# Kernel optimization log

Measured on AMD Instinct MI355X. Metric: run time of the kernel, lower is better.

The kernel has to match this reference:

```python
import jax, jax.numpy as jnp
import numpy as np

B, CIN, COUT, H, W = 64, 2048, 32, 14, 14
REP = 1024


def setup_inputs() -> dict:
    key = jax.random.key(0)
    ks = jax.random.split(key, 7)
    x = jax.random.normal(ks[0], (B, CIN, H, W), dtype=jnp.float32)
    conv_w = jax.random.normal(ks[1], (COUT, CIN, 3, 3), dtype=jnp.float32) * (1.0 / np.sqrt(CIN * 9))
    conv_b = jax.random.normal(ks[2], (COUT,), dtype=jnp.float32) * 0.01
    w6 = jax.random.normal(ks[3], (REP, CIN * COUT), dtype=jnp.float32) * (1.0 / np.sqrt(CIN * COUT))
    b6 = jax.random.normal(ks[4], (REP,), dtype=jnp.float32) * 0.01
    w7 = jax.random.normal(ks[5], (REP, REP), dtype=jnp.float32) * (1.0 / np.sqrt(REP))
    b7 = jax.random.normal(ks[6], (REP,), dtype=jnp.float32) * 0.01
    return {"x": x, "conv_w": conv_w, "conv_b": conv_b,
            "w6": w6, "b6": b6, "w7": w7, "b7": b7}


def reference(x, conv_w, conv_b, w6, b6, w7, b7):
    # attention_map = Conv2d(in->out, k=3, s=1, p=1)(x)  -> [B, COUT, H, W]
    am = jax.lax.conv_general_dilated(
        x, conv_w, window_strides=(1, 1), padding=((1, 1), (1, 1)),
        dimension_numbers=("NCHW", "OIHW", "NCHW"))
    am = am + conv_b[None, :, None, None]
    # outer product am[:,None]*x[:,:,None] followed by AdaptiveAvgPool2d(1)
    # == mean over HW of the product: [B, CIN, COUT]
    hw = x.shape[2] * x.shape[3]
    pooled = jnp.einsum("bihw,bohw->bio", x, am) / hw
    feat = pooled.reshape(pooled.shape[0], -1)          # [B, CIN*COUT]
    h6 = jax.nn.relu(feat @ w6.T + b6)                  # [B, REP]
    out = jax.nn.relu(h6 @ w7.T + b7)                   # [B, REP]
    return out
```

## Files before the change

kernel.cpp:

```cpp
#include <hip/hip_runtime.h>
#include <hip/hip_bf16.h>

#define B_   64
#define CIN  2048
#define COUT 32
#define P    196
#define PPAD 224
#define REP  1024
#define K1   (CIN*COUT)
#define NSL  16

typedef float  f32x4  __attribute__((ext_vector_type(4)));
typedef __bf16 bf16x8 __attribute__((ext_vector_type(8)));
typedef __bf16 bf16x4 __attribute__((ext_vector_type(4)));

#define OFF_W2     0
#define OFF_AMP    1179648
#define OFF_AMBF   30539776
#define OFF_POOLED 31457280
#define OFF_S1     39845888
#define OFF_H6B    48234496
#define OFF_S2     48365568

static __device__ __forceinline__ f32x4 mfma16(bf16x8 a, bf16x8 b, f32x4 c) {
  return __builtin_amdgcn_mfma_f32_16x16x32_bf16(a, b, c, 0, 0, 0);
}

__global__ __launch_bounds__(256)
void prep_w2(const float* __restrict__ cw, __bf16* __restrict__ W2) {
  const int blk = blockIdx.x;
  const int o = blk >> 3, cc = blk & 7;
  const int cin = cc * 256 + threadIdx.x;
  const float* src = cw + ((size_t)o * CIN + cin) * 9;
  #pragma unroll
  for (int d = 0; d < 9; d++)
    W2[((size_t)d * COUT + o) * CIN + cin] = (__bf16)src[d];
}

#define ICW 72
__global__ __launch_bounds__(448)
void conv_kernel(const float* __restrict__ x, const __bf16* __restrict__ W2,
                 float* __restrict__ amp) {
  __shared__ __bf16 XT[256 * ICW];

  const int ksl = blockIdx.x;
  const int bb  = blockIdx.y;
  const int t   = threadIdx.x;
  const int wv  = t >> 6;
  const int lane = t & 63;
  const int q = lane >> 4, ln = lane & 15;
  const float* xb = x + (size_t)bb * CIN * P;
  const int kbase = ksl * 128;

  int rb[2]; bool valid[2]; int pix[2];
  #pragma unroll
  for (int nt = 0; nt < 2; nt++) {
    const int pt = wv * 32 + nt * 16 + ln;
    pix[nt] = pt; valid[nt] = (pt < P);
    const int pr = valid[nt] ? pt : 0;
    const int h = pr / 14, w = pr - (pr / 14) * 14;
    rb[nt] = (h + 1) * 16 + (w + 1);
  }
  f32x4 acc[2][2];
  #pragma unroll
  for (int m = 0; m < 2; m++)
    #pragma unroll
    for (int n = 0; n < 2; n++) { f32x4 z = {0.f,0.f,0.f,0.f}; acc[m][n] = z; }

  const int nIter = (t < 224) ? 4 : 3;
  int obase[4], dst[4];
  #pragma unroll
  for (int it = 0; it < 4; it++) {
    const int u = t + 448 * it;
    if (u < 1568) {
      const int g = u / 196, p = u - g * 196;
      const int h = p / 14, w = p - (p / 14) * 14;
      obase[it] = (g * 8) * P + p;
      dst[it]   = ((h + 1) * 16 + (w + 1)) * ICW + g * 8;
    } else { obase[it] = 0; dst[it] = 0; }
  }

  bf16x8 pre[4];
  #pragma unroll
  for (int it = 0; it < 4; it++)
    if (it < nIter) {
      bf16x8 v;
      #pragma unroll
      for (int j = 0; j < 8; j++)
        v[j] = (__bf16)xb[(size_t)kbase * P + obase[it] + j * P];
      pre[it] = v;
    }

  if (t < 256) {
    const int hh = t >> 4, ww = t & 15;
    if (hh == 0 || hh == 15 || ww == 0 || ww == 15) {
      #pragma unroll
      for (int g = 0; g < 8; g++) { bf16x8 z = {}; *(bf16x8*)&XT[t * ICW + g * 8] = z; }
    }
  }

  #pragma unroll
  for (int it = 0; it < 4; it++)
    if (it < nIter) *(bf16x8*)&XT[dst[it]] = pre[it];

  #pragma unroll
  for (int it = 0; it < 4; it++)
    if (it < nIter) {
      bf16x8 v;
      #pragma unroll
      for (int j = 0; j < 8; j++)
        v[j] = (__bf16)xb[(size_t)(kbase + 64) * P + obase[it] + j * P];
      pre[it] = v;
    }

  __syncthreads();

  #pragma unroll
  for (int sub = 0; sub < 2; sub++) {
    const int i0 = kbase + sub * 64;
    #pragma unroll
    for (int ks2 = 0; ks2 < 2; ks2++) {
      const int kg  = i0 + ks2 * 32 + q * 8;
      const int off = (ks2 * 4 + q) * 8;
      #pragma unroll
      for (int d = 0; d < 9; d++) {
        const int dy = d / 3, dx = d - (d / 3) * 3;
        const int delta = (dy - 1) * 16 + (dx - 1);
        bf16x8 a0 = *(const bf16x8*)&W2[(size_t)(d * COUT + ln) * CIN + kg];
        bf16x8 a1 = *(const bf16x8*)&W2[(size_t)(d * COUT + 16 + ln) * CIN + kg];
        #pragma unroll
        for (int nt = 0; nt < 2; nt++) {
          bf16x8 bf = *(const bf16x8*)&XT[(rb[nt] + delta) * ICW + off];
          acc[0][nt] = mfma16(a0, bf, acc[0][nt]);
          acc[1][nt] = mfma16(a1, bf, acc[1][nt]);
        }
      }
    }
    if (sub == 0) {
      __syncthreads();
      #pragma unroll
      for (int it = 0; it < 4; it++)
        if (it < nIter) *(bf16x8*)&XT[dst[it]] = pre[it];
      __syncthreads();
    }
  }

  float* dstp = amp + (((size_t)ksl * B_ + bb) * COUT) * PPAD;
  #pragma unroll
  for (int mt = 0; mt < 2; mt++)
    #pragma unroll
    for (int nt = 0; nt < 2; nt++)
      if (valid[nt]) {
        #pragma unroll
        for (int r = 0; r < 4; r++) {
          const int o = mt * 16 + q * 4 + r;
          dstp[(size_t)o * PPAD + pix[nt]] = acc[mt][nt][r];
        }
      }
}

__global__ __launch_bounds__(256)
void am_final_kernel(const float* __restrict__ amp, const float* __restrict__ cb,
                     __bf16* __restrict__ am_bf) {
  const int NE = B_ * COUT * PPAD;
  for (int e = blockIdx.x * 256 + threadIdx.x; e < NE; e += 448 * 256) {
    const int row = e / PPAD;
    const int pe  = e - row * PPAD;
    float v = 0.f;
    if (pe < P) {
      float s = 0.f;
      #pragma unroll
      for (int sl = 0; sl < NSL; sl++) s += amp[(size_t)sl * NE + e];
      v = s + cb[row & (COUT - 1)];
    }
    am_bf[e] = (__bf16)v;
  }
}

__global__ __launch_bounds__(256)
void pooled_kernel(const float* __restrict__ x, const __bf16* __restrict__ amb_,
                   __bf16* __restrict__ pooled) {
  const int b  = blockIdx.y;
  const int ig = blockIdx.x;
  const int t  = threadIdx.x;
  const int wv = t >> 6;
  const int lane = t & 63;
  const int q = lane >> 4, ln = lane & 15;
  const int ibase = ig * 128 + wv * 32;

  f32x4 acc[2][2];
  #pragma unroll
  for (int a = 0; a < 2; a++)
    #pragma unroll
    for (int c = 0; c < 2; c++) { f32x4 z = {0.f,0.f,0.f,0.f}; acc[a][c] = z; }

  const __bf16* amb = amb_ + (size_t)b * COUT * PPAD;
  const float*  xb  = x + (size_t)b * CIN * P;

  #pragma unroll
  for (int kc = 0; kc < 7; kc++) {
    const int k0 = kc * 32 + q * 8;
    bf16x8 af[2];
    #pragma unroll
    for (int o2 = 0; o2 < 2; o2++)
      af[o2] = *(const bf16x8*)&amb[(size_t)(o2 * 16 + ln) * PPAD + k0];
    #pragma unroll
    for (int it = 0; it < 2; it++) {
      const int i = ibase + it * 16 + ln;
      bf16x8 bfr;
      if (kc < 6) {
        const float* src = &xb[(size_t)i * P + k0];
        f32x4 v0 = *(const f32x4*)src;
        f32x4 v1 = *(const f32x4*)(src + 4);
        #pragma unroll
        for (int j = 0; j < 4; j++) { bfr[j] = (__bf16)v0[j]; bfr[4 + j] = (__bf16)v1[j]; }
      } else {
        #pragma unroll
        for (int j = 0; j < 8; j++) {
          const int p = k0 + j;
          bfr[j] = (p < P) ? (__bf16)xb[(size_t)i * P + p] : (__bf16)0.f;
        }
      }
      acc[0][it] = mfma16(af[0], bfr, acc[0][it]);
      acc[1][it] = mfma16(af[1], bfr, acc[1][it]);
    }
  }

  const float sc = 1.0f / 196.0f;
  #pragma unroll
  for (int o2 = 0; o2 < 2; o2++)
    #pragma unroll
    for (int it = 0; it < 2; it++) {
      const int i = ibase + it * 16 + ln;
      bf16x4 vv;
      #pragma unroll
      for (int r = 0; r < 4; r++) vv[r] = (__bf16)(acc[o2][it][r] * sc);
      *(bf16x4*)&pooled[(size_t)b * K1 + (size_t)i * COUT + o2 * 16 + q * 4] = vv;
    }
}

__global__ __launch_bounds__(256)
void gemm1_kernel(const __bf16* __restrict__ pooled, const float* __restrict__ w6,
                  float* __restrict__ S1) {
  const int nb = blockIdx.x, ks = blockIdx.y;
  const int t = threadIdx.x;
  const int wv = t >> 6;
  const int lane = t & 63;
  const int q = lane >> 4, ln = lane & 15;
  const int n0 = nb * 64 + wv * 16;
  const int kbase = ks * 2048;

  f32x4 acc[4];
  #pragma unroll
  for (int a = 0; a < 4; a++) { f32x4 z = {0.f,0.f,0.f,0.f}; acc[a] = z; }

  #pragma unroll 4
  for (int kc = 0; kc < 64; kc++) {
    const int k0 = kbase + kc * 32 + q * 8;
    const float* src = &w6[(size_t)(n0 + ln) * K1 + k0];
    f32x4 v0 = *(const f32x4*)src;
    f32x4 v1 = *(const f32x4*)(src + 4);
    bf16x8 bfr;
    #pragma unroll
    for (int j = 0; j < 4; j++) { bfr[j] = (__bf16)v0[j]; bfr[4 + j] = (__bf16)v1[j]; }
    #pragma unroll
    for (int mi = 0; mi < 4; mi++) {
      bf16x8 af = *(const bf16x8*)&pooled[(size_t)(mi * 16 + ln) * K1 + k0];
      acc[mi] = mfma16(af, bfr, acc[mi]);
    }
  }
  #pragma unroll
  for (int mi = 0; mi < 4; mi++)
    #pragma unroll
    for (int r = 0; r < 4; r++)
      S1[(size_t)ks * (B_ * REP) + (size_t)(mi * 16 + q * 4 + r) * REP + n0 + ln] = acc[mi][r];
}

__global__ __launch_bounds__(256)
void reduce1_kernel(const float* __restrict__ S1, const float* __restrict__ b6,
                    __bf16* __restrict__ h6b) {
  const int idx = blockIdx.x * 256 + threadIdx.x;
  float s = 0.f;
  #pragma unroll 8
  for (int ks = 0; ks < 32; ks++) s += S1[(size_t)ks * (B_ * REP) + idx];
  h6b[idx] = (__bf16)fmaxf(s + b6[idx & (REP - 1)], 0.f);
}

__global__ __launch_bounds__(256)
void gemm2_kernel(const __bf16* __restrict__ h6b, const float* __restrict__ w7,
                  float* __restrict__ S2) {
  const int nb = blockIdx.x, ks = blockIdx.y;
  const int t = threadIdx.x;
  const int wv = t >> 6;
  const int lane = t & 63;
  const int q = lane >> 4, ln = lane & 15;
  const int n0 = nb * 64 + wv * 16;

  f32x4 acc[4];
  #pragma unroll
  for (int a = 0; a < 4; a++) { f32x4 z = {0.f,0.f,0.f,0.f}; acc[a] = z; }

  #pragma unroll
  for (int kc = 0; kc < 4; kc++) {
    const int k0 = ks * 128 + kc * 32 + q * 8;
    const float* src = &w7[(size_t)(n0 + ln) * REP + k0];
    f32x4 v0 = *(const f32x4*)src;
    f32x4 v1 = *(const f32x4*)(src + 4);
    bf16x8 bfr;
    #pragma unroll
    for (int j = 0; j < 4; j++) { bfr[j] = (__bf16)v0[j]; bfr[4 + j] = (__bf16)v1[j]; }
    #pragma unroll
    for (int mi = 0; mi < 4; mi++) {
      bf16x8 af = *(const bf16x8*)&h6b[(size_t)(mi * 16 + ln) * REP + k0];
      acc[mi] = mfma16(af, bfr, acc[mi]);
    }
  }
  #pragma unroll
  for (int mi = 0; mi < 4; mi++)
    #pragma unroll
    for (int r = 0; r < 4; r++)
      S2[(size_t)ks * (B_ * REP) + (size_t)(mi * 16 + q * 4 + r) * REP + n0 + ln] = acc[mi][r];
}

__global__ __launch_bounds__(256)
void reduce2_kernel(const float* __restrict__ S2, const float* __restrict__ b7,
                    float* __restrict__ out) {
  const int idx = blockIdx.x * 256 + threadIdx.x;
  float s = 0.f;
  #pragma unroll
  for (int ks = 0; ks < 8; ks++) s += S2[(size_t)ks * (B_ * REP) + idx];
  out[idx] = fmaxf(s + b7[idx & (REP - 1)], 0.f);
}

extern "C" void kernel_launch(void* const* d_in, const int* in_sizes, int n_in,
                              void* d_out, int out_size, void* d_ws, size_t ws_size,
                              hipStream_t stream) {
  const float* x   = (const float*)d_in[0];
  const float* cw  = (const float*)d_in[1];
  const float* cb  = (const float*)d_in[2];
  const float* w6  = (const float*)d_in[3];
  const float* b6  = (const float*)d_in[4];
  const float* w7  = (const float*)d_in[5];
  const float* b7  = (const float*)d_in[6];
  float* out = (float*)d_out;

  char* ws = (char*)d_ws;
  __bf16* W2     = (__bf16*)(ws + OFF_W2);
  float*  amp    = (float*)(ws + OFF_AMP);
  __bf16* am_bf  = (__bf16*)(ws + OFF_AMBF);
  __bf16* pooled = (__bf16*)(ws + OFF_POOLED);
  float*  S1     = (float*)(ws + OFF_S1);
  __bf16* h6b    = (__bf16*)(ws + OFF_H6B);
  float*  S2     = (float*)(ws + OFF_S2);

  prep_w2        <<<256,          256, 0, stream>>>(cw, W2);
  conv_kernel    <<<dim3(16, 64), 448, 0, stream>>>(x, W2, amp);
  am_final_kernel<<<448,          256, 0, stream>>>(amp, cb, am_bf);
  pooled_kernel  <<<dim3(16, 64), 256, 0, stream>>>(x, am_bf, pooled);
  gemm1_kernel   <<<dim3(16, 32), 256, 0, stream>>>(pooled, w6, S1);
  reduce1_kernel <<<256,          256, 0, stream>>>(S1, b6, h6b);
  gemm2_kernel   <<<dim3(16, 8),  256, 0, stream>>>(h6b, w7, S2);
  reduce2_kernel <<<256,          256, 0, stream>>>(S2, b7, out);
}
```

Measured before the change: 572.7 us.

## Load full conv K-slice at once, double gemm1 split-K, fuse gemm2 reduction

The conv kernel now stages all 128 input channels of its slice into a wider LDS tile in one pass, dropping the two-phase double-buffer and its extra barriers. gemm1 uses 64 K-splits instead of 32 for more parallelism, and reduce1 reads the larger partial buffer. gemm2 drops split-K, does the full K loop per block, and applies bias and ReLU directly, which removes reduce2 and the S2 buffer. The trade-offs are more LDS per conv block, lower occupancy, and only 16 blocks for gemm2.

```diff
diff --git a/kernel.cpp b/kernel.cpp
--- a/kernel.cpp
+++ b/kernel.cpp
@@ -19,8 +19,7 @@
 #define OFF_AMBF   30539776
 #define OFF_POOLED 31457280
 #define OFF_S1     39845888
-#define OFF_H6B    48234496
-#define OFF_S2     48365568
+#define OFF_H6B    56623104
 
 static __device__ __forceinline__ f32x4 mfma16(bf16x8 a, bf16x8 b, f32x4 c) {
   return __builtin_amdgcn_mfma_f32_16x16x32_bf16(a, b, c, 0, 0, 0);
@@ -37,11 +36,11 @@
     W2[((size_t)d * COUT + o) * CIN + cin] = (__bf16)src[d];
 }
 
-#define ICW 72
+#define ICW2 136
 __global__ __launch_bounds__(448)
 void conv_kernel(const float* __restrict__ x, const __bf16* __restrict__ W2,
                  float* __restrict__ amp) {
-  __shared__ __bf16 XT[256 * ICW];
+  __shared__ __bf16 XT[256 * ICW2];
 
   const int ksl = blockIdx.x;
   const int bb  = blockIdx.y;
@@ -67,81 +66,63 @@
     #pragma unroll
     for (int n = 0; n < 2; n++) { f32x4 z = {0.f,0.f,0.f,0.f}; acc[m][n] = z; }
 
-  const int nIter = (t < 224) ? 4 : 3;
-  int obase[4], dst[4];
+  int obase[7], dst[7];
+  #pragma unroll
+  for (int it = 0; it < 7; it++) {
+    const int u = t + 448 * it;
+    const int g = u / 196, p = u - g * 196;
+    const int h = p / 14, w = p - (p / 14) * 14;
+    obase[it] = (kbase + g * 8) * P + p;
+    dst[it]   = ((h + 1) * 16 + (w + 1)) * ICW2 + g * 8;
+  }
+
+  bf16x8 pre[4];
   #pragma unroll
   for (int it = 0; it < 4; it++) {
-    const int u = t + 448 * it;
-    if (u < 1568) {
-      const int g = u / 196, p = u - g * 196;
-      const int h = p / 14, w = p - (p / 14) * 14;
-      obase[it] = (g * 8) * P + p;
-      dst[it]   = ((h + 1) * 16 + (w + 1)) * ICW + g * 8;
-    } else { obase[it] = 0; dst[it] = 0; }
-  }
-
-  bf16x8 pre[4];
-  #pragma unroll
-  for (int it = 0; it < 4; it++)
-    if (it < nIter) {
-      bf16x8 v;
-      #pragma unroll
-      for (int j = 0; j < 8; j++)
-        v[j] = (__bf16)xb[(size_t)kbase * P + obase[it] + j * P];
-      pre[it] = v;
-    }
-
+    bf16x8 v;
+    #pragma unroll
+    for (int j = 0; j < 8; j++) v[j] = (__bf16)xb[obase[it] + j * P];
+    pre[it] = v;
+  }
   if (t < 256) {
     const int hh = t >> 4, ww = t & 15;
     if (hh == 0 || hh == 15 || ww == 0 || ww == 15) {
       #pragma unroll
-      for (int g = 0; g < 8; g++) { bf16x8 z = {}; *(bf16x8*)&XT[t * ICW + g * 8] = z; }
-    }
-  }
-
-  #pragma unroll
-  for (int it = 0; it < 4; it++)
-    if (it < nIter) *(bf16x8*)&XT[dst[it]] = pre[it];
-
-  #pragma unroll
-  for (int it = 0; it < 4; it++)
-    if (it < nIter) {
-      bf16x8 v;
+      for (int g = 0; g < 16; g++) { bf16x8 z = {}; *(bf16x8*)&XT[t * ICW2 + g * 8] = z; }
+    }
+  }
+  #pragma unroll
+  for (int it = 0; it < 4; it++) *(bf16x8*)&XT[dst[it]] = pre[it];
+
+  bf16x8 pre2[3];
+  #pragma unroll
+  for (int it = 0; it < 3; it++) {
+    bf16x8 v;
+    #pragma unroll
+    for (int j = 0; j < 8; j++) v[j] = (__bf16)xb[obase[4 + it] + j * P];
+    pre2[it] = v;
+  }
+  #pragma unroll
+  for (int it = 0; it < 3; it++) *(bf16x8*)&XT[dst[4 + it]] = pre2[it];
+
+  __syncthreads();
+
+  #pragma unroll
+  for (int ks2 = 0; ks2 < 4; ks2++) {
+    const int kg  = kbase + ks2 * 32 + q * 8;
+    const int off = (ks2 * 4 + q) * 8;
+    #pragma unroll
+    for (int d = 0; d < 9; d++) {
+      const int dy = d / 3, dx = d - (d / 3) * 3;
+      const int delta = (dy - 1) * 16 + (dx - 1);
+      bf16x8 a0 = *(const bf16x8*)&W2[(size_t)(d * COUT + ln) * CIN + kg];
+      bf16x8 a1 = *(const bf16x8*)&W2[(size_t)(d * COUT + 16 + ln) * CIN + kg];
       #pragma unroll
-      for (int j = 0; j < 8; j++)
-        v[j] = (__bf16)xb[(size_t)(kbase + 64) * P + obase[it] + j * P];
-      pre[it] = v;
-    }
-
-  __syncthreads();
-
-  #pragma unroll
-  for (int sub = 0; sub < 2; sub++) {
-    const int i0 = kbase + sub * 64;
-    #pragma unroll
-    for (int ks2 = 0; ks2 < 2; ks2++) {
-      const int kg  = i0 + ks2 * 32 + q * 8;
-      const int off = (ks2 * 4 + q) * 8;
-      #pragma unroll
-      for (int d = 0; d < 9; d++) {
-        const int dy = d / 3, dx = d - (d / 3) * 3;
-        const int delta = (dy - 1) * 16 + (dx - 1);
-        bf16x8 a0 = *(const bf16x8*)&W2[(size_t)(d * COUT + ln) * CIN + kg];
-        bf16x8 a1 = *(const bf16x8*)&W2[(size_t)(d * COUT + 16 + ln) * CIN + kg];
-        #pragma unroll
-        for (int nt = 0; nt < 2; nt++) {
-          bf16x8 bf = *(const bf16x8*)&XT[(rb[nt] + delta) * ICW + off];
-          acc[0][nt] = mfma16(a0, bf, acc[0][nt]);
-          acc[1][nt] = mfma16(a1, bf, acc[1][nt]);
-        }
+      for (int nt = 0; nt < 2; nt++) {
+        bf16x8 bf = *(const bf16x8*)&XT[(rb[nt] + delta) * ICW2 + off];
+        acc[0][nt] = mfma16(a0, bf, acc[0][nt]);
+        acc[1][nt] = mfma16(a1, bf, acc[1][nt]);
       }
-    }
-    if (sub == 0) {
-      __syncthreads();
-      #pragma unroll
-      for (int it = 0; it < 4; it++)
-        if (it < nIter) *(bf16x8*)&XT[dst[it]] = pre[it];
-      __syncthreads();
     }
   }
 
@@ -248,14 +229,14 @@
   const int lane = t & 63;
   const int q = lane >> 4, ln = lane & 15;
   const int n0 = nb * 64 + wv * 16;
-  const int kbase = ks * 2048;
+  const int kbase = ks * 1024;
 
   f32x4 acc[4];
   #pragma unroll
   for (int a = 0; a < 4; a++) { f32x4 z = {0.f,0.f,0.f,0.f}; acc[a] = z; }
 
   #pragma unroll 4
-  for (int kc = 0; kc < 64; kc++) {
+  for (int kc = 0; kc < 32; kc++) {
     const int k0 = kbase + kc * 32 + q * 8;
     const float* src = &w6[(size_t)(n0 + ln) * K1 + k0];
     f32x4 v0 = *(const f32x4*)src;
@@ -282,14 +263,14 @@
   const int idx = blockIdx.x * 256 + threadIdx.x;
   float s = 0.f;
   #pragma unroll 8
-  for (int ks = 0; ks < 32; ks++) s += S1[(size_t)ks * (B_ * REP) + idx];
+  for (int ks = 0; ks < 64; ks++) s += S1[(size_t)ks * (B_ * REP) + idx];
   h6b[idx] = (__bf16)fmaxf(s + b6[idx & (REP - 1)], 0.f);
 }
 
 __global__ __launch_bounds__(256)
 void gemm2_kernel(const __bf16* __restrict__ h6b, const float* __restrict__ w7,
-                  float* __restrict__ S2) {
-  const int nb = blockIdx.x, ks = blockIdx.y;
+                  const float* __restrict__ b7, float* __restrict__ out) {
+  const int nb = blockIdx.x;
   const int t = threadIdx.x;
   const int wv = t >> 6;
   const int lane = t & 63;
@@ -300,9 +281,9 @@
   #pragma unroll
   for (int a = 0; a < 4; a++) { f32x4 z = {0.f,0.f,0.f,0.f}; acc[a] = z; }
 
-  #pragma unroll
-  for (int kc = 0; kc < 4; kc++) {
-    const int k0 = ks * 128 + kc * 32 + q * 8;
+  #pragma unroll 4
+  for (int kc = 0; kc < 32; kc++) {
+    const int k0 = kc * 32 + q * 8;
     const float* src = &w7[(size_t)(n0 + ln) * REP + k0];
     f32x4 v0 = *(const f32x4*)src;
     f32x4 v1 = *(const f32x4*)(src + 4);
@@ -315,21 +296,13 @@
       acc[mi] = mfma16(af, bfr, acc[mi]);
     }
   }
+
+  const float bias = b7[n0 + ln];
   #pragma unroll
   for (int mi = 0; mi < 4; mi++)
     #pragma unroll
     for (int r = 0; r < 4; r++)
-      S2[(size_t)ks * (B_ * REP) + (size_t)(mi * 16 + q * 4 + r) * REP + n0 + ln] = acc[mi][r];
-}
-
-__global__ __launch_bounds__(256)
-void reduce2_kernel(const float* __restrict__ S2, const float* __restrict__ b7,
-                    float* __restrict__ out) {
-  const int idx = blockIdx.x * 256 + threadIdx.x;
-  float s = 0.f;
-  #pragma unroll
-  for (int ks = 0; ks < 8; ks++) s += S2[(size_t)ks * (B_ * REP) + idx];
-  out[idx] = fmaxf(s + b7[idx & (REP - 1)], 0.f);
+      out[(size_t)(mi * 16 + q * 4 + r) * REP + n0 + ln] = fmaxf(acc[mi][r] + bias, 0.f);
 }
 
 extern "C" void kernel_launch(void* const* d_in, const int* in_sizes, int n_in,
@@ -351,14 +324,12 @@
   __bf16* pooled = (__bf16*)(ws + OFF_POOLED);
   float*  S1     = (float*)(ws + OFF_S1);
   __bf16* h6b    = (__bf16*)(ws + OFF_H6B);
-  float*  S2     = (float*)(ws + OFF_S2);
 
   prep_w2        <<<256,          256, 0, stream>>>(cw, W2);
   conv_kernel    <<<dim3(16, 64), 448, 0, stream>>>(x, W2, amp);
   am_final_kernel<<<448,          256, 0, stream>>>(amp, cb, am_bf);
   pooled_kernel  <<<dim3(16, 64), 256, 0, stream>>>(x, am_bf, pooled);
-  gemm1_kernel   <<<dim3(16, 32), 256, 0, stream>>>(pooled, w6, S1);
+  gemm1_kernel   <<<dim3(16, 64), 256, 0, stream>>>(pooled, w6, S1);
   reduce1_kernel <<<256,          256, 0, stream>>>(S1, b6, h6b);
-  gemm2_kernel   <<<dim3(16, 8),  256, 0, stream>>>(h6b, w7, S2);
-  reduce2_kernel <<<256,          256, 0, stream>>>(S2, b7, out);
-}
+  gemm2_kernel   <<<16,           256, 0, stream>>>(h6b, w7, b7, out);
+}
```

After: 600.9 us. +4.9%, slower.

## Replace conv split-K partial buffer with atomics and fuse reductions into consumers

Applied to the files above, without the earlier changes.

Conv slices now atomically accumulate into a single zeroed activation map instead of writing 16 partial copies, so the separate reduction kernel is removed and the bias is added inside the pooling kernel. The second GEMM drops its K split and applies bias and ReLU directly, eliminating the final reduction kernel. This cuts large intermediate memory traffic and two launches, at the cost of atomic contention and a much smaller grid for the second GEMM.

```diff
diff --git a/kernel.cpp b/kernel.cpp
--- a/kernel.cpp
+++ b/kernel.cpp
@@ -15,12 +15,10 @@
 typedef __bf16 bf16x4 __attribute__((ext_vector_type(4)));
 
 #define OFF_W2     0
-#define OFF_AMP    1179648
-#define OFF_AMBF   30539776
-#define OFF_POOLED 31457280
-#define OFF_S1     39845888
-#define OFF_H6B    48234496
-#define OFF_S2     48365568
+#define OFF_AM     1310720
+#define OFF_POOLED 3145728
+#define OFF_S1     11534336
+#define OFF_H6B    19922944
 
 static __device__ __forceinline__ f32x4 mfma16(bf16x8 a, bf16x8 b, f32x4 c) {
   return __builtin_amdgcn_mfma_f32_16x16x32_bf16(a, b, c, 0, 0, 0);
@@ -40,7 +38,7 @@
 #define ICW 72
 __global__ __launch_bounds__(448)
 void conv_kernel(const float* __restrict__ x, const __bf16* __restrict__ W2,
-                 float* __restrict__ amp) {
+                 float* __restrict__ am) {
   __shared__ __bf16 XT[256 * ICW];
 
   const int ksl = blockIdx.x;
@@ -145,7 +143,6 @@
     }
   }
 
-  float* dstp = amp + (((size_t)ksl * B_ + bb) * COUT) * PPAD;
   #pragma unroll
   for (int mt = 0; mt < 2; mt++)
     #pragma unroll
@@ -154,32 +151,14 @@
         #pragma unroll
         for (int r = 0; r < 4; r++) {
           const int o = mt * 16 + q * 4 + r;
-          dstp[(size_t)o * PPAD + pix[nt]] = acc[mt][nt][r];
+          atomicAdd(&am[((size_t)bb * COUT + o) * PPAD + pix[nt]], acc[mt][nt][r]);
         }
       }
 }
 
 __global__ __launch_bounds__(256)
-void am_final_kernel(const float* __restrict__ amp, const float* __restrict__ cb,
-                     __bf16* __restrict__ am_bf) {
-  const int NE = B_ * COUT * PPAD;
-  for (int e = blockIdx.x * 256 + threadIdx.x; e < NE; e += 448 * 256) {
-    const int row = e / PPAD;
-    const int pe  = e - row * PPAD;
-    float v = 0.f;
-    if (pe < P) {
-      float s = 0.f;
-      #pragma unroll
-      for (int sl = 0; sl < NSL; sl++) s += amp[(size_t)sl * NE + e];
-      v = s + cb[row & (COUT - 1)];
-    }
-    am_bf[e] = (__bf16)v;
-  }
-}
-
-__global__ __launch_bounds__(256)
-void pooled_kernel(const float* __restrict__ x, const __bf16* __restrict__ amb_,
-                   __bf16* __restrict__ pooled) {
+void pooled_kernel(const float* __restrict__ x, const float* __restrict__ amp,
+                   const float* __restrict__ cb, __bf16* __restrict__ pooled) {
   const int b  = blockIdx.y;
   const int ig = blockIdx.x;
   const int t  = threadIdx.x;
@@ -194,16 +173,24 @@
     #pragma unroll
     for (int c = 0; c < 2; c++) { f32x4 z = {0.f,0.f,0.f,0.f}; acc[a][c] = z; }
 
-  const __bf16* amb = amb_ + (size_t)b * COUT * PPAD;
-  const float*  xb  = x + (size_t)b * CIN * P;
+  const float* amb = amp + (size_t)b * COUT * PPAD;
+  const float* xb  = x + (size_t)b * CIN * P;
+  const float cbv[2] = { cb[ln], cb[16 + ln] };
 
   #pragma unroll
   for (int kc = 0; kc < 7; kc++) {
     const int k0 = kc * 32 + q * 8;
     bf16x8 af[2];
     #pragma unroll
-    for (int o2 = 0; o2 < 2; o2++)
-      af[o2] = *(const bf16x8*)&amb[(size_t)(o2 * 16 + ln) * PPAD + k0];
+    for (int o2 = 0; o2 < 2; o2++) {
+      const float* src = &amb[(size_t)(o2 * 16 + ln) * PPAD + k0];
+      f32x4 v0 = *(const f32x4*)src;
+      f32x4 v1 = *(const f32x4*)(src + 4);
+      bf16x8 a;
+      #pragma unroll
+      for (int j = 0; j < 4; j++) { a[j] = (__bf16)(v0[j] + cbv[o2]); a[4 + j] = (__bf16)(v1[j] + cbv[o2]); }
+      af[o2] = a;
+    }
     #pragma unroll
     for (int it = 0; it < 2; it++) {
       const int i = ibase + it * 16 + ln;
@@ -281,15 +268,15 @@
                     __bf16* __restrict__ h6b) {
   const int idx = blockIdx.x * 256 + threadIdx.x;
   float s = 0.f;
-  #pragma unroll 8
+  #pragma unroll
   for (int ks = 0; ks < 32; ks++) s += S1[(size_t)ks * (B_ * REP) + idx];
   h6b[idx] = (__bf16)fmaxf(s + b6[idx & (REP - 1)], 0.f);
 }
 
 __global__ __launch_bounds__(256)
 void gemm2_kernel(const __bf16* __restrict__ h6b, const float* __restrict__ w7,
-                  float* __restrict__ S2) {
-  const int nb = blockIdx.x, ks = blockIdx.y;
+                  const float* __restrict__ b7, float* __restrict__ out) {
+  const int nb = blockIdx.x;
   const int t = threadIdx.x;
   const int wv = t >> 6;
   const int lane = t & 63;
@@ -300,9 +287,9 @@
   #pragma unroll
   for (int a = 0; a < 4; a++) { f32x4 z = {0.f,0.f,0.f,0.f}; acc[a] = z; }
 
-  #pragma unroll
-  for (int kc = 0; kc < 4; kc++) {
-    const int k0 = ks * 128 + kc * 32 + q * 8;
+  #pragma unroll 4
+  for (int kc = 0; kc < 32; kc++) {
+    const int k0 = kc * 32 + q * 8;
     const float* src = &w7[(size_t)(n0 + ln) * REP + k0];
     f32x4 v0 = *(const f32x4*)src;
     f32x4 v1 = *(const f32x4*)(src + 4);
@@ -315,21 +302,13 @@
       acc[mi] = mfma16(af, bfr, acc[mi]);
     }
   }
+
+  const float bias = b7[n0 + ln];
   #pragma unroll
   for (int mi = 0; mi < 4; mi++)
     #pragma unroll
     for (int r = 0; r < 4; r++)
-      S2[(size_t)ks * (B_ * REP) + (size_t)(mi * 16 + q * 4 + r) * REP + n0 + ln] = acc[mi][r];
-}
-
-__global__ __launch_bounds__(256)
-void reduce2_kernel(const float* __restrict__ S2, const float* __restrict__ b7,
-                    float* __restrict__ out) {
-  const int idx = blockIdx.x * 256 + threadIdx.x;
-  float s = 0.f;
-  #pragma unroll
-  for (int ks = 0; ks < 8; ks++) s += S2[(size_t)ks * (B_ * REP) + idx];
-  out[idx] = fmaxf(s + b7[idx & (REP - 1)], 0.f);
+      out[(size_t)(mi * 16 + q * 4 + r) * REP + n0 + ln] = fmaxf(acc[mi][r] + bias, 0.f);
 }
 
 extern "C" void kernel_launch(void* const* d_in, const int* in_sizes, int n_in,
@@ -346,19 +325,16 @@
 
   char* ws = (char*)d_ws;
   __bf16* W2     = (__bf16*)(ws + OFF_W2);
-  float*  amp    = (float*)(ws + OFF_AMP);
-  __bf16* am_bf  = (__bf16*)(ws + OFF_AMBF);
+  float*  am     = (float*)(ws + OFF_AM);
   __bf16* pooled = (__bf16*)(ws + OFF_POOLED);
   float*  S1     = (float*)(ws + OFF_S1);
   __bf16* h6b    = (__bf16*)(ws + OFF_H6B);
-  float*  S2     = (float*)(ws + OFF_S2);
-
-  prep_w2        <<<256,          256, 0, stream>>>(cw, W2);
-  conv_kernel    <<<dim3(16, 64), 448, 0, stream>>>(x, W2, amp);
-  am_final_kernel<<<448,          256, 0, stream>>>(amp, cb, am_bf);
-  pooled_kernel  <<<dim3(16, 64), 256, 0, stream>>>(x, am_bf, pooled);
-  gemm1_kernel   <<<dim3(16, 32), 256, 0, stream>>>(pooled, w6, S1);
-  reduce1_kernel <<<256,          256, 0, stream>>>(S1, b6, h6b);
-  gemm2_kernel   <<<dim3(16, 8),  256, 0, stream>>>(h6b, w7, S2);
-  reduce2_kernel <<<256,          256, 0, stream>>>(S2, b7, out);
-}
+
+  hipMemsetAsync(am, 0, (size_t)B_ * COUT * PPAD * 4, stream);
+  prep_w2       <<<256,          256, 0, stream>>>(cw, W2);
+  conv_kernel   <<<dim3(16, 64), 448, 0, stream>>>(x, W2, am);
+  pooled_kernel <<<dim3(16, 64), 256, 0, stream>>>(x, am, cb, pooled);
+  gemm1_kernel  <<<dim3(16, 32), 256, 0, stream>>>(pooled, w6, S1);
+  reduce1_kernel<<<256,          256, 0, stream>>>(S1, b6, h6b);
+  gemm2_kernel  <<<16,           256, 0, stream>>>(h6b, w7, b7, out);
+}
```

Measured after the change: 600.8 us. 4.9% more time.
